# Kernel optimization log

Measured on AMD Instinct MI355X. Metric: run time of the kernel, lower is better.

## Reference

```python
import jax, jax.numpy as jnp
import numpy as np


def setup_inputs() -> dict:
    key = jax.random.key(0)
    k1, k2 = jax.random.split(key, 2)
    B, T, C = 8, 2048, 1024
    x = jax.random.normal(k1, (B, T, C), dtype=jnp.float32)
    # nn.Linear weight, scaled like default init ~U(-1/sqrt(C), 1/sqrt(C)); use scaled normal
    W = jax.random.normal(k2, (C, C), dtype=jnp.float32) * (1.0 / np.sqrt(C))
    b = jnp.zeros((C,), dtype=jnp.float32)
    return {"x": x, "W": W, "b": b}


def reference(x, W, b):
    # v = Linear(x): torch stores weight as [out, in], y = x @ W.T + b
    v = jnp.einsum("btc,dc->btd", x, W) + b  # [B,T,C]
    B, T, C = x.shape
    # attn_mask has ones only in column 1, so bmm(mask, v) == broadcast v[:,1,:]
    # (T > 1 here by construction; T == 1 case would return v directly)
    y = jnp.broadcast_to(v[:, 1:2, :], (B, T, C))
    return y
```

## Files before the change

### kernel.cpp

```cpp
#include <hip/hip_runtime.h>
#include <hip/hip_bf16.h>


#define B_  8
#define T_  2048
#define C_  1024

__global__ __launch_bounds__(256) void gemv_row1(
    const float* __restrict__ x, const float* __restrict__ W,
    const float* __restrict__ bias, float* __restrict__ v1) {
    const int wave = blockIdx.x * (blockDim.x >> 6) + (threadIdx.x >> 6);
    const int lane = threadIdx.x & 63;
    const int b = wave >> 10;
    const int d = wave & (C_ - 1);
    if (b >= B_) return;

    const float4* __restrict__ xr = reinterpret_cast<const float4*>(
        x + (size_t)b * T_ * C_ + C_);
    const float4* __restrict__ wr = reinterpret_cast<const float4*>(
        W + (size_t)d * C_);

    float sum = 0.f;
    #pragma unroll
    for (int k = lane; k < C_ / 4; k += 64) {
        float4 a = xr[k];
        float4 w = wr[k];
        sum += a.x * w.x + a.y * w.y + a.z * w.z + a.w * w.w;
    }
    #pragma unroll
    for (int off = 32; off > 0; off >>= 1)
        sum += __shfl_xor(sum, off, 64);

    if (lane == 0) v1[wave] = sum + bias[d];
}

__global__ __launch_bounds__(256) void bcast_row(
    const float4* __restrict__ v4, float4* __restrict__ out4) {
    const int i = blockIdx.x * blockDim.x + threadIdx.x;
    const int b  = i >> 19;
    const int d4 = i & 255;
    out4[i] = v4[(b << 8) + d4];
}

extern "C" void kernel_launch(void* const* d_in, const int* in_sizes, int n_in,
                              void* d_out, int out_size, void* d_ws, size_t ws_size,
                              hipStream_t stream) {
    const float* x    = (const float*)d_in[0];
    const float* W    = (const float*)d_in[1];
    const float* bias = (const float*)d_in[2];
    float* out = (float*)d_out;
    float* v1  = (float*)d_ws;

    gemv_row1<<<(B_ * C_) / 4, 256, 0, stream>>>(x, W, bias, v1);

    const int total4 = B_ * T_ * C_ / 4;
    bcast_row<<<total4 / 256, 256, 0, stream>>>(
        (const float4*)v1, (float4*)out);
}
```

Measured before the change: 111.9 us.

## Fuse GEMV and broadcast into one kernel with per-block output tiles

Merges the row-1 GEMV and the broadcast write into a single kernel. Each of 256 blocks computes 32 output features for one batch (8 threads per feature), stages them in shared memory, then writes those 32 columns across all 2048 time steps. This removes a kernel launch and the workspace round trip. In exchange, only 256 blocks do the 64MB write, with each thread writing 32-byte strided chunks rather than fully contiguous rows, which may reduce write bandwidth.

```diff
diff --git a/kernel.cpp b/kernel.cpp
--- a/kernel.cpp
+++ b/kernel.cpp
@@ -6,40 +6,49 @@
 #define T_  2048
 #define C_  1024
 
-__global__ __launch_bounds__(256) void gemv_row1(
+__global__ __launch_bounds__(256) void fused_target_attn(
     const float* __restrict__ x, const float* __restrict__ W,
-    const float* __restrict__ bias, float* __restrict__ v1) {
-    const int wave = blockIdx.x * (blockDim.x >> 6) + (threadIdx.x >> 6);
-    const int lane = threadIdx.x & 63;
-    const int b = wave >> 10;
-    const int d = wave & (C_ - 1);
-    if (b >= B_) return;
+    const float* __restrict__ bias, float* __restrict__ out) {
+    __shared__ float v_s[32];
+
+    const int bid = blockIdx.x;
+    const int b   = bid >> 5;
+    const int d0  = (bid & 31) << 5;
+
+    const int tid = threadIdx.x;
+    const int row = tid >> 3;
+    const int sub = tid & 7;
 
     const float4* __restrict__ xr = reinterpret_cast<const float4*>(
         x + (size_t)b * T_ * C_ + C_);
     const float4* __restrict__ wr = reinterpret_cast<const float4*>(
-        W + (size_t)d * C_);
+        W + (size_t)(d0 + row) * C_);
 
-    float sum = 0.f;
+    float s = 0.f;
     #pragma unroll
-    for (int k = lane; k < C_ / 4; k += 64) {
+    for (int i = 0; i < 32; ++i) {
+        const int k = sub + (i << 3);
         float4 a = xr[k];
         float4 w = wr[k];
-        sum += a.x * w.x + a.y * w.y + a.z * w.z + a.w * w.w;
+        s += a.x * w.x + a.y * w.y + a.z * w.z + a.w * w.w;
     }
-    #pragma unroll
-    for (int off = 32; off > 0; off >>= 1)
-        sum += __shfl_xor(sum, off, 64);
+    s += __shfl_xor(s, 1, 64);
+    s += __shfl_xor(s, 2, 64);
+    s += __shfl_xor(s, 4, 64);
+    if (sub == 0) v_s[row] = s + bias[d0 + row];
+    __syncthreads();
 
-    if (lane == 0) v1[wave] = sum + bias[d];
-}
+    const int t_sub = tid >> 3;
+    const int d4    = tid & 7;
+    const float4 val = reinterpret_cast<const float4*>(v_s)[d4];
 
-__global__ __launch_bounds__(256) void bcast_row(
-    const float4* __restrict__ v4, float4* __restrict__ out4) {
-    const int i = blockIdx.x * blockDim.x + threadIdx.x;
-    const int b  = i >> 19;
-    const int d4 = i & 255;
-    out4[i] = v4[(b << 8) + d4];
+    float4* __restrict__ out4 = reinterpret_cast<float4*>(out);
+    size_t idx = ((size_t)b << 19) + ((size_t)t_sub << 8) + (d0 >> 2) + d4;
+    #pragma unroll 8
+    for (int k = 0; k < 64; ++k) {
+        out4[idx] = val;
+        idx += 8192;
+    }
 }
 
 extern "C" void kernel_launch(void* const* d_in, const int* in_sizes, int n_in,
@@ -49,11 +58,6 @@
     const float* W    = (const float*)d_in[1];
     const float* bias = (const float*)d_in[2];
     float* out = (float*)d_out;
-    float* v1  = (float*)d_ws;
 
-    gemv_row1<<<(B_ * C_) / 4, 256, 0, stream>>>(x, W, bias, v1);
-
-    const int total4 = B_ * T_ * C_ / 4;
-    bcast_row<<<total4 / 256, 256, 0, stream>>>(
-        (const float4*)v1, (float4*)out);
+    fused_target_attn<<<256, 256, 0, stream>>>(x, W, bias, out);
 }
```

Measured after the change: 109.2 us. -2.4%, faster.
